# Performance work log

Measured on AMD Instinct MI355X. Metric: run time of the kernel, lower is better.

Reference implementation:

```python
import jax, jax.numpy as jnp
import numpy as np

N_NODES = 50000
N_EDGES = 1600000
NEG_SLOPE = 0.2


def setup_inputs() -> dict:
    key = jax.random.key(0)
    ks = jax.random.split(key, 11)
    s = 0.1  # small init scale
    return {
        "x": jax.random.normal(ks[0], (N_NODES, 128), dtype=jnp.float32),
        "edge_index": jax.random.randint(ks[1], (2, N_EDGES), 0, N_NODES, dtype=jnp.int64),
        "W1": jax.random.normal(ks[2], (128, 128), dtype=jnp.float32) * s,
        "att_src1": jax.random.normal(ks[3], (2, 64), dtype=jnp.float32) * s,
        "att_dst1": jax.random.normal(ks[4], (2, 64), dtype=jnp.float32) * s,
        "b1": jax.random.normal(ks[5], (128,), dtype=jnp.float32) * s,
        "W2": jax.random.normal(ks[6], (128, 64), dtype=jnp.float32) * s,
        "att_src2": jax.random.normal(ks[7], (1, 64), dtype=jnp.float32) * s,
        "att_dst2": jax.random.normal(ks[8], (1, 64), dtype=jnp.float32) * s,
        "b2": jax.random.normal(ks[9], (64,), dtype=jnp.float32) * s,
    }


def gat_conv(x, W, a_src, a_dst, bias, src, dst, n_nodes):
    # x: [N, F_in]; W: [F_in, H*C]; a_src/a_dst: [H, C]; bias: [H*C]
    H, C = a_src.shape
    xl = (x @ W).reshape(n_nodes, H, C)                 # [N,H,C]
    alpha_s = jnp.einsum('nhc,hc->nh', xl, a_src)       # [N,H]
    alpha_d = jnp.einsum('nhc,hc->nh', xl, a_dst)       # [N,H]
    e = jax.nn.leaky_relu(alpha_s[src] + alpha_d[dst], NEG_SLOPE)  # [E,H]
    # segment softmax over edges sharing the same destination node
    m = jax.ops.segment_max(e, dst, num_segments=n_nodes)          # [N,H]
    m = jnp.where(jnp.isfinite(m), m, 0.0)
    e = jnp.exp(e - m[dst])
    denom = jax.ops.segment_sum(e, dst, num_segments=n_nodes)      # [N,H]
    alpha = e / denom[dst]                               # self-loops guarantee denom > 0
    msg = xl[src] * alpha[:, :, None]                    # [E,H,C]
    out = jax.ops.segment_sum(msg, dst, num_segments=n_nodes)      # [N,H,C]
    return out.reshape(n_nodes, H * C) + bias


def reference(x, edge_index, W1, att_src1, att_dst1, b1, W2, att_src2, att_dst2, b2):
    n = x.shape[0]
    # PyG GATConv default add_self_loops=True
    loops = jnp.arange(n, dtype=edge_index.dtype)
    src = jnp.concatenate([edge_index[0], loops])
    dst = jnp.concatenate([edge_index[1], loops])

    h = gat_conv(x, W1, att_src1, att_dst1, b1, src, dst, n)   # [N, 128]
    h = jax.nn.relu(h)                                          # dropout p=0 (eval)
    h = gat_conv(h, W2, att_src2, att_dst2, b2, src, dst, n)   # [N, 64]
    h = jax.nn.relu(h)
    return h
```

## Files before the change

### kernel.cpp

```cpp
#include <hip/hip_runtime.h>
#include <cstdint>
#include <cstddef>

#define NEG_SLOPE 0.2f

#define NB 128
#define LOG_NB 7
#define MAXK 512

__device__ inline unsigned short f2bf(float f) {
    unsigned int u = __float_as_uint(f);
    u += 0x7FFFu + ((u >> 16) & 1u);
    return (unsigned short)(u >> 16);
}
__device__ inline float bf_lo(unsigned int u) { return __uint_as_float(u << 16); }
__device__ inline float bf_hi(unsigned int u) { return __uint_as_float(u & 0xFFFF0000u); }

__global__ __launch_bounds__(256) void sort_count_kernel(const int* __restrict__ ei, int E,
                                                         int K, int CH, int* __restrict__ bcnt) {
    __shared__ int hist[4 * MAXK];
    int tid = threadIdx.x;
    int wiw = tid >> 6;
    for (int i = tid; i < K; i += 256) {
        hist[i] = 0; hist[MAXK + i] = 0; hist[2 * MAXK + i] = 0; hist[3 * MAXK + i] = 0;
    }
    __syncthreads();
    int lo = blockIdx.x * CH;
    int hi = lo + CH; if (hi > E) hi = E;
    for (int e = lo + tid; e < hi; e += 256)
        atomicAdd(&hist[wiw * MAXK + (ei[(size_t)E + e] >> LOG_NB)], 1);
    __syncthreads();
    for (int i = tid; i < K; i += 256) {
        int c = hist[i] + hist[MAXK + i] + hist[2 * MAXK + i] + hist[3 * MAXK + i];
        if (c) atomicAdd(&bcnt[i], c);
    }
}

__global__ void sort_scan_kernel(const int* __restrict__ bcnt, int* __restrict__ boff,
                                 int* __restrict__ bcur, int K, int E) {
    __shared__ int buf[MAXK];
    int tid = threadIdx.x;
    int v = (tid < K) ? bcnt[tid] : 0;
    buf[tid] = v;
    __syncthreads();
    for (int o = 1; o < MAXK; o <<= 1) {
        int t = (tid >= o) ? buf[tid - o] : 0;
        __syncthreads();
        buf[tid] += t;
        __syncthreads();
    }
    if (tid < K) {
        int ex = buf[tid] - v;
        boff[tid] = ex;
        bcur[tid] = ex;
    }
    if (tid == K) boff[K] = E;
}


template <int FOUT, int H, int ROWS>
__device__ __forceinline__ void gemm_att_body(const float* __restrict__ X,
                                              const float* __restrict__ W,
                                              const float* __restrict__ attS,
                                              const float* __restrict__ attD,
                                              unsigned short* __restrict__ Ybf,
                                              float* __restrict__ as_,
                                              float* __restrict__ ad_, int N, int bid,
                                              float* sX, float* sW) {
    constexpr int CG  = FOUT / 4;
    constexpr int RR  = (ROWS * FOUT) / 1024;
    constexpr int LDX = 36;
    int tid = threadIdx.x;
    int rowbase = bid * ROWS;
    int cg = tid % CG;
    int rg = tid / CG;
    int r0 = rg * RR;

    float acc[RR][4];
#pragma unroll
    for (int i = 0; i < RR; i++)
#pragma unroll
        for (int c = 0; c < 4; c++) acc[i][c] = 0.f;

    for (int k0 = 0; k0 < 128; k0 += 32) {
        __syncthreads();
        for (int idx = tid; idx < ROWS * 8; idx += 256) {
            int r = idx >> 3, q = idx & 7;
            int row = rowbase + r;
            float4 val = (row < N) ? *(const float4*)&X[(size_t)row * 128 + k0 + q * 4]
                                   : make_float4(0.f, 0.f, 0.f, 0.f);
            *(float4*)&sX[r * LDX + q * 4] = val;
        }
        for (int idx = tid; idx < 8 * FOUT; idx += 256)
            *(float4*)&sW[idx * 4] = *(const float4*)&W[(size_t)k0 * FOUT + idx * 4];
        __syncthreads();
        for (int k = 0; k < 32; k += 4) {
            float4 xr[RR];
#pragma unroll
            for (int i = 0; i < RR; i++)
                xr[i] = *(const float4*)&sX[(r0 + i) * LDX + k];
#pragma unroll
            for (int kk = 0; kk < 4; kk++) {
                float4 wv = ((const float4*)(sW + (size_t)(k + kk) * FOUT))[cg];
#pragma unroll
                for (int i = 0; i < RR; i++) {
                    float xv = (&xr[i].x)[kk];
                    acc[i][0] = fmaf(xv, wv.x, acc[i][0]);
                    acc[i][1] = fmaf(xv, wv.y, acc[i][1]);
                    acc[i][2] = fmaf(xv, wv.z, acc[i][2]);
                    acc[i][3] = fmaf(xv, wv.w, acc[i][3]);
                }
            }
        }
    }

#pragma unroll
    for (int i = 0; i < RR; i++) {
        int row = rowbase + r0 + i;
        if (row < N) {
            ushort4 v;
            v.x = f2bf(acc[i][0]); v.y = f2bf(acc[i][1]);
            v.z = f2bf(acc[i][2]); v.w = f2bf(acc[i][3]);
            *(ushort4*)(Ybf + (size_t)row * FOUT + cg * 4) = v;
        }
    }

    float4 asv = ((const float4*)attS)[cg];
    float4 adv = ((const float4*)attD)[cg];
    int head = (H == 2) ? (cg >> 4) : 0;
#pragma unroll
    for (int i = 0; i < RR; i++) {
        float ps = acc[i][0] * asv.x + acc[i][1] * asv.y + acc[i][2] * asv.z + acc[i][3] * asv.w;
        float pd = acc[i][0] * adv.x + acc[i][1] * adv.y + acc[i][2] * adv.z + acc[i][3] * adv.w;
#pragma unroll
        for (int o = 1; o <= 8; o <<= 1) { ps += __shfl_xor(ps, o); pd += __shfl_xor(pd, o); }
        int row = rowbase + r0 + i;
        if ((tid & 15) == 0 && row < N) {
            as_[(size_t)row * H + head] = ps;
            ad_[(size_t)row * H + head] = pd;
        }
    }
}

__global__ __launch_bounds__(256) void scatter_gemm1_kernel(const int* __restrict__ ei, int E,
                                                            int K, int CH, int* __restrict__ bcur,
                                                            unsigned int* __restrict__ bkt,
                                                            const float* __restrict__ X,
                                                            const float* __restrict__ W1,
                                                            const float* __restrict__ attS,
                                                            const float* __restrict__ attD,
                                                            unsigned short* __restrict__ Ybf,
                                                            float* __restrict__ as_,
                                                            float* __restrict__ ad_, int N, int G) {
    __shared__ float sX[64 * 36];
    __shared__ float sW[32 * 128];
    if (blockIdx.x < G) {
        int* hist = (int*)sX;
        int* base = (int*)sW;
        int* cur2 = (int*)sW + MAXK;
        int tid = threadIdx.x;
        int wiw = tid >> 6;
        for (int i = tid; i < K; i += 256) {
            hist[i] = 0; hist[MAXK + i] = 0; hist[2 * MAXK + i] = 0; hist[3 * MAXK + i] = 0;
        }
        __syncthreads();
        int lo = blockIdx.x * CH;
        int hi = lo + CH; if (hi > E) hi = E;
        for (int e = lo + tid; e < hi; e += 256)
            atomicAdd(&hist[wiw * MAXK + (ei[(size_t)E + e] >> LOG_NB)], 1);
        __syncthreads();
        for (int i = tid; i < K; i += 256) {
            int c = hist[i] + hist[MAXK + i] + hist[2 * MAXK + i] + hist[3 * MAXK + i];
            base[i] = c ? atomicAdd(&bcur[i], c) : 0;
            cur2[i] = 0;
        }
        __syncthreads();
        for (int e = lo + tid; e < hi; e += 256) {
            int s = ei[e];
            int d = ei[(size_t)E + e];
            int k = d >> LOG_NB;
            int r = atomicAdd(&cur2[k], 1);
            bkt[(size_t)base[k] + r] = (unsigned int)s | ((unsigned int)d << 16);
        }
    } else {
        gemm_att_body<128, 2, 64>(X, W1, attS, attD, Ybf, as_, ad_, N, blockIdx.x - G, sX, sW);
    }
}

__global__ __launch_bounds__(256) void gemm2_kernel(const float* __restrict__ X,
                                                    const float* __restrict__ W,
                                                    const float* __restrict__ attS,
                                                    const float* __restrict__ attD,
                                                    unsigned short* __restrict__ Ybf,
                                                    float* __restrict__ as_,
                                                    float* __restrict__ ad_, int N) {
    __shared__ float sX[64 * 36];
    __shared__ float sW[32 * 64];
    gemm_att_body<64, 1, 64>(X, W, attS, attD, Ybf, as_, ad_, N, blockIdx.x, sX, sW);
}

__global__ __launch_bounds__(256) void sort_finalize_kernel(const unsigned int* __restrict__ bkt,
                                                            const int* __restrict__ boff,
                                                            int* __restrict__ off,
                                                            unsigned int* __restrict__ csrc, int N) {
    __shared__ int nhist[4 * NB];
    __shared__ int part[256];
    __shared__ int loff[NB];
    int k = blockIdx.x;
    int tid = threadIdx.x;
    int wiw = tid >> 6;
    int node0 = k << LOG_NB;
    int nh = N - node0; if (nh > NB) nh = NB;
    int beg = boff[k], end = boff[k + 1];
    for (int i = tid; i < NB; i += 256) {
        nhist[i] = 0; nhist[NB + i] = 0; nhist[2 * NB + i] = 0; nhist[3 * NB + i] = 0;
    }
    __syncthreads();
    for (int e = beg + tid; e < end; e += 256)
        atomicAdd(&nhist[wiw * NB + ((bkt[e] >> 16) - node0)], 1);
    __syncthreads();
    int i0 = 2 * tid, i1 = 2 * tid + 1;
    int v0 = (i0 < nh) ? nhist[i0] + nhist[NB + i0] + nhist[2 * NB + i0] + nhist[3 * NB + i0] + 1 : 0;
    int v1 = (i1 < nh) ? nhist[i1] + nhist[NB + i1] + nhist[2 * NB + i1] + nhist[3 * NB + i1] + 1 : 0;
    part[tid] = v0 + v1;
    __syncthreads();
    for (int o = 1; o < 256; o <<= 1) {
        int t = (tid >= o) ? part[tid - o] : 0;
        __syncthreads();
        part[tid] += t;
        __syncthreads();
    }
    int gbase = beg + node0;
    int base = gbase + ((tid > 0) ? part[tid - 1] : 0);
    if (i0 < nh) loff[i0] = base;
    if (i1 < nh) loff[i1] = base + v0;
    __syncthreads();
    for (int i = tid; i < nh; i += 256) {
        int node = node0 + i;
        off[node] = loff[i];
        csrc[loff[i]] = (unsigned int)node | ((unsigned int)node << 16);
        nhist[i] = loff[i] + 1;
    }
    if (node0 + nh == N && tid == 0) off[N] = gbase + part[255];
    __syncthreads();
    for (int e = beg + tid; e < end; e += 256) {
        unsigned int p = bkt[e];
        int pos = atomicAdd(&nhist[(p >> 16) - node0], 1);
        csrc[pos] = p;
    }
}


__global__ __launch_bounds__(256) void agg1_kernel(const unsigned short* __restrict__ xl,
                                                   const float* __restrict__ as_,
                                                   const float* __restrict__ ad_,
                                                   const float* __restrict__ bias,
                                                   const int* __restrict__ off,
                                                   const unsigned int* __restrict__ csrc,
                                                   float* __restrict__ out, int N) {
    __shared__ float4 sps[4][64];
    int wiw  = threadIdx.x >> 6;
    int lane = threadIdx.x & 63;
    int node = blockIdx.x * 4 + wiw;
    if (node >= N) return;
    int beg = off[node], end = off[node + 1];
    int deg = end - beg;
    float2 adn = ((const float2*)ad_)[node];

    int cl  = lane & 15;
    int sub = lane >> 4;
    int hd1 = (cl >> 3) & 1;
    float acc[8];
#pragma unroll
    for (int i = 0; i < 8; i++) acc[i] = 0.f;
    const char* xbase = (const char*)xl + cl * 16;

    if (deg <= 64) {
        int so = 0;
        float t0 = -1e30f, t1 = -1e30f;
        if (lane < deg) {
            int s = (int)(csrc[beg + lane] & 0xFFFFu);
            so = s << 8;
            float2 asv = ((const float2*)as_)[s];
            t0 = asv.x + adn.x; t0 = t0 > 0.f ? t0 : NEG_SLOPE * t0;
            t1 = asv.y + adn.y; t1 = t1 > 0.f ? t1 : NEG_SLOPE * t1;
        }
        float m0 = t0, m1 = t1;
#pragma unroll
        for (int o = 32; o; o >>= 1) {
            m0 = fmaxf(m0, __shfl_xor(m0, o));
            m1 = fmaxf(m1, __shfl_xor(m1, o));
        }
        float e0 = (lane < deg) ? __expf(t0 - m0) : 0.f;
        float e1 = (lane < deg) ? __expf(t1 - m1) : 0.f;
        float s0 = e0, s1 = e1;
#pragma unroll
        for (int o = 32; o; o >>= 1) { s0 += __shfl_xor(s0, o); s1 += __shfl_xor(s1, o); }
        sps[wiw][lane] = make_float4(e0 / s0, e1 / s1, __int_as_float(so), 0.f);
        int iters = (deg + 3) >> 2;
#pragma unroll 8
        for (int j = 0; j < iters; j++) {
            float4 q = sps[wiw][j * 4 + sub];
            float a  = hd1 ? q.y : q.x;
            uint4 v  = *(const uint4*)(xbase + __float_as_int(q.z));
            acc[0] = fmaf(a, bf_lo(v.x), acc[0]); acc[1] = fmaf(a, bf_hi(v.x), acc[1]);
            acc[2] = fmaf(a, bf_lo(v.y), acc[2]); acc[3] = fmaf(a, bf_hi(v.y), acc[3]);
            acc[4] = fmaf(a, bf_lo(v.z), acc[4]); acc[5] = fmaf(a, bf_hi(v.z), acc[5]);
            acc[6] = fmaf(a, bf_lo(v.w), acc[6]); acc[7] = fmaf(a, bf_hi(v.w), acc[7]);
        }
    } else {
        float m0 = -1e30f, m1 = -1e30f;
        for (int b = beg; b < end; b += 64) {
            int e = b + lane;
            if (e < end) {
                int s = (int)(csrc[e] & 0xFFFFu);
                float2 asv = ((const float2*)as_)[s];
                float t0 = asv.x + adn.x; t0 = t0 > 0.f ? t0 : NEG_SLOPE * t0;
                float t1 = asv.y + adn.y; t1 = t1 > 0.f ? t1 : NEG_SLOPE * t1;
                m0 = fmaxf(m0, t0); m1 = fmaxf(m1, t1);
            }
        }
#pragma unroll
        for (int o = 32; o; o >>= 1) {
            m0 = fmaxf(m0, __shfl_xor(m0, o));
            m1 = fmaxf(m1, __shfl_xor(m1, o));
        }
        float s0 = 0.f, s1 = 0.f;
        for (int b = beg; b < end; b += 64) {
            int e = b + lane;
            if (e < end) {
                int s = (int)(csrc[e] & 0xFFFFu);
                float2 asv = ((const float2*)as_)[s];
                float t0 = asv.x + adn.x; t0 = t0 > 0.f ? t0 : NEG_SLOPE * t0;
                float t1 = asv.y + adn.y; t1 = t1 > 0.f ? t1 : NEG_SLOPE * t1;
                s0 += __expf(t0 - m0); s1 += __expf(t1 - m1);
            }
        }
#pragma unroll
        for (int o = 32; o; o >>= 1) { s0 += __shfl_xor(s0, o); s1 += __shfl_xor(s1, o); }
        float i0 = 1.f / s0, i1 = 1.f / s1;
        for (int b = beg; b < end; b += 64) {
            int cnt = end - b; if (cnt > 64) cnt = 64;
            float p0 = 0.f, p1 = 0.f; int so = 0;
            if (lane < cnt) {
                int s = (int)(csrc[b + lane] & 0xFFFFu);
                so = s << 8;
                float2 asv = ((const float2*)as_)[s];
                float t0 = asv.x + adn.x; t0 = t0 > 0.f ? t0 : NEG_SLOPE * t0;
                float t1 = asv.y + adn.y; t1 = t1 > 0.f ? t1 : NEG_SLOPE * t1;
                p0 = __expf(t0 - m0) * i0; p1 = __expf(t1 - m1) * i1;
            }
            sps[wiw][lane] = make_float4(p0, p1, __int_as_float(so), 0.f);
            int iters = (cnt + 3) >> 2;
#pragma unroll 8
            for (int j = 0; j < iters; j++) {
                float4 q = sps[wiw][j * 4 + sub];
                float a  = hd1 ? q.y : q.x;
                uint4 v  = *(const uint4*)(xbase + __float_as_int(q.z));
                acc[0] = fmaf(a, bf_lo(v.x), acc[0]); acc[1] = fmaf(a, bf_hi(v.x), acc[1]);
                acc[2] = fmaf(a, bf_lo(v.y), acc[2]); acc[3] = fmaf(a, bf_hi(v.y), acc[3]);
                acc[4] = fmaf(a, bf_lo(v.z), acc[4]); acc[5] = fmaf(a, bf_hi(v.z), acc[5]);
                acc[6] = fmaf(a, bf_lo(v.w), acc[6]); acc[7] = fmaf(a, bf_hi(v.w), acc[7]);
            }
        }
    }
#pragma unroll
    for (int o = 16; o <= 32; o <<= 1)
#pragma unroll
        for (int i = 0; i < 8; i++) acc[i] += __shfl_xor(acc[i], o);
    if (sub == 0) {
        float* op = out + (size_t)node * 128 + cl * 8;
        const float* bp = bias + cl * 8;
#pragma unroll
        for (int i = 0; i < 8; i++) op[i] = fmaxf(acc[i] + bp[i], 0.f);
    }
}


__global__ __launch_bounds__(256) void agg2_kernel(const unsigned short* __restrict__ xl,
                                                   const float* __restrict__ as_,
                                                   const float* __restrict__ ad_,
                                                   const float* __restrict__ bias,
                                                   const int* __restrict__ off,
                                                   const unsigned int* __restrict__ csrc,
                                                   float* __restrict__ out, int N) {
    __shared__ float2 sps[4][64];
    int wiw  = threadIdx.x >> 6;
    int lane = threadIdx.x & 63;
    int node = blockIdx.x * 4 + wiw;
    if (node >= N) return;
    int beg = off[node], end = off[node + 1];
    int deg = end - beg;
    float adn = ad_[node];

    int cl  = lane & 7;
    int sub = lane >> 3;
    float acc[8];
#pragma unroll
    for (int i = 0; i < 8; i++) acc[i] = 0.f;
    const char* xbase = (const char*)xl + cl * 16;

    if (deg <= 64) {
        int so = 0;
        float t = -1e30f;
        if (lane < deg) {
            int s = (int)(csrc[beg + lane] & 0xFFFFu);
            so = s << 7;
            t = as_[s] + adn;
            t = t > 0.f ? t : NEG_SLOPE * t;
        }
        float m = t;
#pragma unroll
        for (int o = 32; o; o >>= 1) m = fmaxf(m, __shfl_xor(m, o));
        float evv = (lane < deg) ? __expf(t - m) : 0.f;
        float sum = evv;
#pragma unroll
        for (int o = 32; o; o >>= 1) sum += __shfl_xor(sum, o);
        sps[wiw][lane] = make_float2(evv / sum, __int_as_float(so));
        int iters = (deg + 7) >> 3;
#pragma unroll 8
        for (int j = 0; j < iters; j++) {
            float2 q = sps[wiw][j * 8 + sub];
            float a  = q.x;
            uint4 v  = *(const uint4*)(xbase + __float_as_int(q.y));
            acc[0] = fmaf(a, bf_lo(v.x), acc[0]); acc[1] = fmaf(a, bf_hi(v.x), acc[1]);
            acc[2] = fmaf(a, bf_lo(v.y), acc[2]); acc[3] = fmaf(a, bf_hi(v.y), acc[3]);
            acc[4] = fmaf(a, bf_lo(v.z), acc[4]); acc[5] = fmaf(a, bf_hi(v.z), acc[5]);
            acc[6] = fmaf(a, bf_lo(v.w), acc[6]); acc[7] = fmaf(a, bf_hi(v.w), acc[7]);
        }
    } else {
        float m = -1e30f;
        for (int b = beg; b < end; b += 64) {
            int e = b + lane;
            if (e < end) {
                float t = as_[csrc[e] & 0xFFFFu] + adn;
                t = t > 0.f ? t : NEG_SLOPE * t;
                m = fmaxf(m, t);
            }
        }
#pragma unroll
        for (int o = 32; o; o >>= 1) m = fmaxf(m, __shfl_xor(m, o));
        float sum = 0.f;
        for (int b = beg; b < end; b += 64) {
            int e = b + lane;
            if (e < end) {
                float t = as_[csrc[e] & 0xFFFFu] + adn;
                t = t > 0.f ? t : NEG_SLOPE * t;
                sum += __expf(t - m);
            }
        }
#pragma unroll
        for (int o = 32; o; o >>= 1) sum += __shfl_xor(sum, o);
        float inv = 1.f / sum;
        for (int b = beg; b < end; b += 64) {
            int cnt = end - b; if (cnt > 64) cnt = 64;
            float p = 0.f; int so = 0;
            if (lane < cnt) {
                int s = (int)(csrc[b + lane] & 0xFFFFu);
                so = s << 7;
                float t = as_[s] + adn;
                t = t > 0.f ? t : NEG_SLOPE * t;
                p = __expf(t - m) * inv;
            }
            sps[wiw][lane] = make_float2(p, __int_as_float(so));
            int iters = (cnt + 7) >> 3;
#pragma unroll 8
            for (int j = 0; j < iters; j++) {
                float2 q = sps[wiw][j * 8 + sub];
                float a  = q.x;
                uint4 v  = *(const uint4*)(xbase + __float_as_int(q.y));
                acc[0] = fmaf(a, bf_lo(v.x), acc[0]); acc[1] = fmaf(a, bf_hi(v.x), acc[1]);
                acc[2] = fmaf(a, bf_lo(v.y), acc[2]); acc[3] = fmaf(a, bf_hi(v.y), acc[3]);
                acc[4] = fmaf(a, bf_lo(v.z), acc[4]); acc[5] = fmaf(a, bf_hi(v.z), acc[5]);
                acc[6] = fmaf(a, bf_lo(v.w), acc[6]); acc[7] = fmaf(a, bf_hi(v.w), acc[7]);
            }
        }
    }
#pragma unroll
    for (int o = 8; o <= 32; o <<= 1)
#pragma unroll
        for (int i = 0; i < 8; i++) acc[i] += __shfl_xor(acc[i], o);
    if (sub == 0) {
        float* op = out + (size_t)node * 64 + cl * 8;
        const float* bp = bias + cl * 8;
#pragma unroll
        for (int i = 0; i < 8; i++) op[i] = fmaxf(acc[i] + bp[i], 0.f);
    }
}


extern "C" void kernel_launch(void* const* d_in, const int* in_sizes, int n_in,
                              void* d_out, int out_size, void* d_ws, size_t ws_size,
                              hipStream_t stream) {
    const float* x        = (const float*)d_in[0];
    const int*   ei       = (const int*)d_in[1];
    const float* W1       = (const float*)d_in[2];
    const float* attS1    = (const float*)d_in[3];
    const float* attD1    = (const float*)d_in[4];
    const float* b1       = (const float*)d_in[5];
    const float* W2       = (const float*)d_in[6];
    const float* attS2    = (const float*)d_in[7];
    const float* attD2    = (const float*)d_in[8];
    const float* b2       = (const float*)d_in[9];
    float* out            = (float*)d_out;

    int N  = in_sizes[0] / 128;
    int E  = in_sizes[1] / 2;
    int EE = E + N;
    int K  = (N + NB - 1) >> LOG_NB;

    char* w = (char*)d_ws;
    auto alloc = [&](size_t bytes) -> void* {
        void* p = (void*)w;
        w += (bytes + 255) & ~(size_t)255;
        return p;
    };
    int*   bcnt = (int*)alloc((size_t)(K + 1) * 4);
    int*   boff = (int*)alloc((size_t)(K + 1) * 4);
    int*   bcur = (int*)alloc((size_t)(K + 1) * 4);
    int*   off  = (int*)alloc((size_t)(N + 1) * 4);
    unsigned int* csrc = (unsigned int*)alloc((size_t)EE * 4);
    unsigned int* bkt  = (unsigned int*)alloc((size_t)E * 4);
    unsigned short* xl1 = (unsigned short*)alloc((size_t)N * 128 * 2);
    float* sd1  = (float*)alloc((size_t)N * 2 * 4);
    float* dd1  = (float*)alloc((size_t)N * 2 * 4);
    float* h1   = (float*)alloc((size_t)N * 128 * 4);

    unsigned short* xl2 = xl1;
    float* sd2 = sd1;
    float* dd2 = dd1;

    hipMemsetAsync(bcnt, 0, (size_t)(K + 1) * 4, stream);

    int G   = 256;
    int CH  = (E + G - 1) / G;
    int GB1 = (N + 63) / 64;
    sort_count_kernel<<<G, 256, 0, stream>>>(ei, E, K, CH, bcnt);
    sort_scan_kernel<<<1, MAXK, 0, stream>>>(bcnt, boff, bcur, K, E);
    scatter_gemm1_kernel<<<G + GB1, 256, 0, stream>>>(ei, E, K, CH, bcur, bkt,
                                                      x, W1, attS1, attD1, xl1, sd1, dd1, N, G);
    sort_finalize_kernel<<<K, 256, 0, stream>>>(bkt, boff, off, csrc, N);

    agg1_kernel<<<(N + 3) / 4, 256, 0, stream>>>(xl1, sd1, dd1, b1, off, csrc, h1, N);

    gemm2_kernel<<<(N + 63) / 64, 256, 0, stream>>>(h1, W2, attS2, attD2, xl2, sd2, dd2, N);
    agg2_kernel<<<(N + 3) / 4, 256, 0, stream>>>(xl2, sd2, dd2, b2, off, csrc, out, N);
}
```

Measured before the change: 298.9 us.

## Process four destination nodes per wavefront with batched softmax prologue loads

New measurement: 321.0 us. +7.4%, slower.

```diff
diff --git a/kernel.cpp b/kernel.cpp
--- a/kernel.cpp
+++ b/kernel.cpp
@@ -250,6 +250,12 @@
     }
 }
 
+#define FMA8(a, v)                                                                       \
+    acc[0] = fmaf(a, bf_lo((v).x), acc[0]); acc[1] = fmaf(a, bf_hi((v).x), acc[1]);      \
+    acc[2] = fmaf(a, bf_lo((v).y), acc[2]); acc[3] = fmaf(a, bf_hi((v).y), acc[3]);      \
+    acc[4] = fmaf(a, bf_lo((v).z), acc[4]); acc[5] = fmaf(a, bf_hi((v).z), acc[5]);      \
+    acc[6] = fmaf(a, bf_lo((v).w), acc[6]); acc[7] = fmaf(a, bf_hi((v).w), acc[7]);
+
 
 __global__ __launch_bounds__(256) void agg1_kernel(const unsigned short* __restrict__ xl,
                                                    const float* __restrict__ as_,
@@ -258,32 +264,46 @@
                                                    const int* __restrict__ off,
                                                    const unsigned int* __restrict__ csrc,
                                                    float* __restrict__ out, int N) {
-    __shared__ float4 sps[4][64];
+    __shared__ float4 sps[4][4][64];
     int wiw  = threadIdx.x >> 6;
     int lane = threadIdx.x & 63;
-    int node = blockIdx.x * 4 + wiw;
-    if (node >= N) return;
-    int beg = off[node], end = off[node + 1];
-    int deg = end - beg;
-    float2 adn = ((const float2*)ad_)[node];
+    int node0 = blockIdx.x * 16 + wiw * 4;
+    if (node0 >= N) return;
 
     int cl  = lane & 15;
     int sub = lane >> 4;
     int hd1 = (cl >> 3) & 1;
-    float acc[8];
-#pragma unroll
-    for (int i = 0; i < 8; i++) acc[i] = 0.f;
     const char* xbase = (const char*)xl + cl * 16;
 
-    if (deg <= 64) {
-        int so = 0;
+    int begk[4], degk[4];
+#pragma unroll
+    for (int k = 0; k < 4; k++) {
+        int node = node0 + k;
+        if (node < N) { int b = off[node]; begk[k] = b; degk[k] = off[node + 1] - b; }
+        else          { begk[k] = 0; degk[k] = 0; }
+    }
+    float2 adnk[4];
+#pragma unroll
+    for (int k = 0; k < 4; k++) {
+        int node = node0 + k;
+        adnk[k] = (node < N) ? ((const float2*)ad_)[node] : make_float2(0.f, 0.f);
+    }
+    int sk[4];
+#pragma unroll
+    for (int k = 0; k < 4; k++)
+        sk[k] = (degk[k] <= 64 && lane < degk[k]) ? (int)(csrc[begk[k] + lane] & 0xFFFFu) : 0;
+    float2 asvk[4];
+#pragma unroll
+    for (int k = 0; k < 4; k++)
+        asvk[k] = ((const float2*)as_)[sk[k]];
+
+#pragma unroll
+    for (int k = 0; k < 4; k++) {
+        if (degk[k] == 0 || degk[k] > 64) continue;
         float t0 = -1e30f, t1 = -1e30f;
-        if (lane < deg) {
-            int s = (int)(csrc[beg + lane] & 0xFFFFu);
-            so = s << 8;
-            float2 asv = ((const float2*)as_)[s];
-            t0 = asv.x + adn.x; t0 = t0 > 0.f ? t0 : NEG_SLOPE * t0;
-            t1 = asv.y + adn.y; t1 = t1 > 0.f ? t1 : NEG_SLOPE * t1;
+        if (lane < degk[k]) {
+            t0 = asvk[k].x + adnk[k].x; t0 = t0 > 0.f ? t0 : NEG_SLOPE * t0;
+            t1 = asvk[k].y + adnk[k].y; t1 = t1 > 0.f ? t1 : NEG_SLOPE * t1;
         }
         float m0 = t0, m1 = t1;
 #pragma unroll
@@ -291,88 +311,95 @@
             m0 = fmaxf(m0, __shfl_xor(m0, o));
             m1 = fmaxf(m1, __shfl_xor(m1, o));
         }
-        float e0 = (lane < deg) ? __expf(t0 - m0) : 0.f;
-        float e1 = (lane < deg) ? __expf(t1 - m1) : 0.f;
+        float e0 = (lane < degk[k]) ? __expf(t0 - m0) : 0.f;
+        float e1 = (lane < degk[k]) ? __expf(t1 - m1) : 0.f;
         float s0 = e0, s1 = e1;
 #pragma unroll
         for (int o = 32; o; o >>= 1) { s0 += __shfl_xor(s0, o); s1 += __shfl_xor(s1, o); }
-        sps[wiw][lane] = make_float4(e0 / s0, e1 / s1, __int_as_float(so), 0.f);
-        int iters = (deg + 3) >> 2;
-#pragma unroll 8
-        for (int j = 0; j < iters; j++) {
-            float4 q = sps[wiw][j * 4 + sub];
-            float a  = hd1 ? q.y : q.x;
-            uint4 v  = *(const uint4*)(xbase + __float_as_int(q.z));
-            acc[0] = fmaf(a, bf_lo(v.x), acc[0]); acc[1] = fmaf(a, bf_hi(v.x), acc[1]);
-            acc[2] = fmaf(a, bf_lo(v.y), acc[2]); acc[3] = fmaf(a, bf_hi(v.y), acc[3]);
-            acc[4] = fmaf(a, bf_lo(v.z), acc[4]); acc[5] = fmaf(a, bf_hi(v.z), acc[5]);
-            acc[6] = fmaf(a, bf_lo(v.w), acc[6]); acc[7] = fmaf(a, bf_hi(v.w), acc[7]);
-        }
-    } else {
-        float m0 = -1e30f, m1 = -1e30f;
-        for (int b = beg; b < end; b += 64) {
-            int e = b + lane;
-            if (e < end) {
-                int s = (int)(csrc[e] & 0xFFFFu);
-                float2 asv = ((const float2*)as_)[s];
-                float t0 = asv.x + adn.x; t0 = t0 > 0.f ? t0 : NEG_SLOPE * t0;
-                float t1 = asv.y + adn.y; t1 = t1 > 0.f ? t1 : NEG_SLOPE * t1;
-                m0 = fmaxf(m0, t0); m1 = fmaxf(m1, t1);
-            }
-        }
-#pragma unroll
-        for (int o = 32; o; o >>= 1) {
-            m0 = fmaxf(m0, __shfl_xor(m0, o));
-            m1 = fmaxf(m1, __shfl_xor(m1, o));
-        }
-        float s0 = 0.f, s1 = 0.f;
-        for (int b = beg; b < end; b += 64) {
-            int e = b + lane;
-            if (e < end) {
-                int s = (int)(csrc[e] & 0xFFFFu);
-                float2 asv = ((const float2*)as_)[s];
-                float t0 = asv.x + adn.x; t0 = t0 > 0.f ? t0 : NEG_SLOPE * t0;
-                float t1 = asv.y + adn.y; t1 = t1 > 0.f ? t1 : NEG_SLOPE * t1;
-                s0 += __expf(t0 - m0); s1 += __expf(t1 - m1);
-            }
-        }
-#pragma unroll
-        for (int o = 32; o; o >>= 1) { s0 += __shfl_xor(s0, o); s1 += __shfl_xor(s1, o); }
-        float i0 = 1.f / s0, i1 = 1.f / s1;
-        for (int b = beg; b < end; b += 64) {
-            int cnt = end - b; if (cnt > 64) cnt = 64;
-            float p0 = 0.f, p1 = 0.f; int so = 0;
-            if (lane < cnt) {
-                int s = (int)(csrc[b + lane] & 0xFFFFu);
-                so = s << 8;
-                float2 asv = ((const float2*)as_)[s];
-                float t0 = asv.x + adn.x; t0 = t0 > 0.f ? t0 : NEG_SLOPE * t0;
-                float t1 = asv.y + adn.y; t1 = t1 > 0.f ? t1 : NEG_SLOPE * t1;
-                p0 = __expf(t0 - m0) * i0; p1 = __expf(t1 - m1) * i1;
-            }
-            sps[wiw][lane] = make_float4(p0, p1, __int_as_float(so), 0.f);
-            int iters = (cnt + 3) >> 2;
+        sps[wiw][k][lane] = make_float4(e0 / s0, e1 / s1, __int_as_float(sk[k] << 8), 0.f);
+    }
+
+#pragma unroll
+    for (int k = 0; k < 4; k++) {
+        int node = node0 + k;
+        if (node >= N) break;
+        float acc[8];
+#pragma unroll
+        for (int i = 0; i < 8; i++) acc[i] = 0.f;
+
+        if (degk[k] <= 64) {
+            int iters = (degk[k] + 3) >> 2;
 #pragma unroll 8
             for (int j = 0; j < iters; j++) {
-                float4 q = sps[wiw][j * 4 + sub];
+                float4 q = sps[wiw][k][j * 4 + sub];
                 float a  = hd1 ? q.y : q.x;
                 uint4 v  = *(const uint4*)(xbase + __float_as_int(q.z));
-                acc[0] = fmaf(a, bf_lo(v.x), acc[0]); acc[1] = fmaf(a, bf_hi(v.x), acc[1]);
-                acc[2] = fmaf(a, bf_lo(v.y), acc[2]); acc[3] = fmaf(a, bf_hi(v.y), acc[3]);
-                acc[4] = fmaf(a, bf_lo(v.z), acc[4]); acc[5] = fmaf(a, bf_hi(v.z), acc[5]);
-                acc[6] = fmaf(a, bf_lo(v.w), acc[6]); acc[7] = fmaf(a, bf_hi(v.w), acc[7]);
-            }
-        }
-    }
-#pragma unroll
-    for (int o = 16; o <= 32; o <<= 1)
-#pragma unroll
-        for (int i = 0; i < 8; i++) acc[i] += __shfl_xor(acc[i], o);
-    if (sub == 0) {
-        float* op = out + (size_t)node * 128 + cl * 8;
-        const float* bp = bias + cl * 8;
-#pragma unroll
-        for (int i = 0; i < 8; i++) op[i] = fmaxf(acc[i] + bp[i], 0.f);
+                FMA8(a, v)
+            }
+        } else {
+            int beg = begk[k], end = beg + degk[k];
+            float m0 = -1e30f, m1 = -1e30f;
+            for (int b = beg; b < end; b += 64) {
+                int e = b + lane;
+                if (e < end) {
+                    int s = (int)(csrc[e] & 0xFFFFu);
+                    float2 asv = ((const float2*)as_)[s];
+                    float t0 = asv.x + adnk[k].x; t0 = t0 > 0.f ? t0 : NEG_SLOPE * t0;
+                    float t1 = asv.y + adnk[k].y; t1 = t1 > 0.f ? t1 : NEG_SLOPE * t1;
+                    m0 = fmaxf(m0, t0); m1 = fmaxf(m1, t1);
+                }
+            }
+#pragma unroll
+            for (int o = 32; o; o >>= 1) {
+                m0 = fmaxf(m0, __shfl_xor(m0, o));
+                m1 = fmaxf(m1, __shfl_xor(m1, o));
+            }
+            float s0 = 0.f, s1 = 0.f;
+            for (int b = beg; b < end; b += 64) {
+                int e = b + lane;
+                if (e < end) {
+                    int s = (int)(csrc[e] & 0xFFFFu);
+                    float2 asv = ((const float2*)as_)[s];
+                    float t0 = asv.x + adnk[k].x; t0 = t0 > 0.f ? t0 : NEG_SLOPE * t0;
+                    float t1 = asv.y + adnk[k].y; t1 = t1 > 0.f ? t1 : NEG_SLOPE * t1;
+                    s0 += __expf(t0 - m0); s1 += __expf(t1 - m1);
+                }
+            }
+#pragma unroll
+            for (int o = 32; o; o >>= 1) { s0 += __shfl_xor(s0, o); s1 += __shfl_xor(s1, o); }
+            float i0 = 1.f / s0, i1 = 1.f / s1;
+            for (int b = beg; b < end; b += 64) {
+                int cnt = end - b; if (cnt > 64) cnt = 64;
+                float p0 = 0.f, p1 = 0.f; int so = 0;
+                if (lane < cnt) {
+                    int s = (int)(csrc[b + lane] & 0xFFFFu);
+                    so = s << 8;
+                    float2 asv = ((const float2*)as_)[s];
+                    float t0 = asv.x + adnk[k].x; t0 = t0 > 0.f ? t0 : NEG_SLOPE * t0;
+                    float t1 = asv.y + adnk[k].y; t1 = t1 > 0.f ? t1 : NEG_SLOPE * t1;
+                    p0 = __expf(t0 - m0) * i0; p1 = __expf(t1 - m1) * i1;
+                }
+                sps[wiw][k][lane] = make_float4(p0, p1, __int_as_float(so), 0.f);
+                int iters = (cnt + 3) >> 2;
+#pragma unroll 8
+                for (int j = 0; j < iters; j++) {
+                    float4 q = sps[wiw][k][j * 4 + sub];
+                    float a  = hd1 ? q.y : q.x;
+                    uint4 v  = *(const uint4*)(xbase + __float_as_int(q.z));
+                    FMA8(a, v)
+                }
+            }
+        }
+#pragma unroll
+        for (int o = 16; o <= 32; o <<= 1)
+#pragma unroll
+            for (int i = 0; i < 8; i++) acc[i] += __shfl_xor(acc[i], o);
+        if (sub == 0) {
+            float* op = out + (size_t)node * 128 + cl * 8;
+            const float* bp = bias + cl * 8;
+#pragma unroll
+            for (int i = 0; i < 8; i++) op[i] = fmaxf(acc[i] + bp[i], 0.f);
+        }
     }
 }
 
@@ -384,107 +411,129 @@
                                                    const int* __restrict__ off,
                                                    const unsigned int* __restrict__ csrc,
                                                    float* __restrict__ out, int N) {
-    __shared__ float2 sps[4][64];
+    __shared__ float2 sps[4][4][64];
     int wiw  = threadIdx.x >> 6;
     int lane = threadIdx.x & 63;
-    int node = blockIdx.x * 4 + wiw;
-    if (node >= N) return;
-    int beg = off[node], end = off[node + 1];
-    int deg = end - beg;
-    float adn = ad_[node];
+    int node0 = blockIdx.x * 16 + wiw * 4;
+    if (node0 >= N) return;
 
     int cl  = lane & 7;
     int sub = lane >> 3;
-    float acc[8];
-#pragma unroll
-    for (int i = 0; i < 8; i++) acc[i] = 0.f;
     const char* xbase = (const char*)xl + cl * 16;
 
-    if (deg <= 64) {
-        int so = 0;
+    int begk[4], degk[4];
+#pragma unroll
+    for (int k = 0; k < 4; k++) {
+        int node = node0 + k;
+        if (node < N) { int b = off[node]; begk[k] = b; degk[k] = off[node + 1] - b; }
+        else          { begk[k] = 0; degk[k] = 0; }
+    }
+    float adnk[4];
+#pragma unroll
+    for (int k = 0; k < 4; k++) {
+        int node = node0 + k;
+        adnk[k] = (node < N) ? ad_[node] : 0.f;
+    }
+    int sk[4];
+#pragma unroll
+    for (int k = 0; k < 4; k++)
+        sk[k] = (degk[k] <= 64 && lane < degk[k]) ? (int)(csrc[begk[k] + lane] & 0xFFFFu) : 0;
+    float asvk[4];
+#pragma unroll
+    for (int k = 0; k < 4; k++)
+        asvk[k] = as_[sk[k]];
+
+#pragma unroll
+    for (int k = 0; k < 4; k++) {
+        if (degk[k] == 0 || degk[k] > 64) continue;
         float t = -1e30f;
-        if (lane < deg) {
-            int s = (int)(csrc[beg + lane] & 0xFFFFu);
-            so = s << 7;
-            t = as_[s] + adn;
+        if (lane < degk[k]) {
+            t = asvk[k] + adnk[k];
             t = t > 0.f ? t : NEG_SLOPE * t;
         }
         float m = t;
 #pragma unroll
         for (int o = 32; o; o >>= 1) m = fmaxf(m, __shfl_xor(m, o));
-        float evv = (lane < deg) ? __expf(t - m) : 0.f;
+        float evv = (lane < degk[k]) ? __expf(t - m) : 0.f;
         float sum = evv;
 #pragma unroll
         for (int o = 32; o; o >>= 1) sum += __shfl_xor(sum, o);
-        sps[wiw][lane] = make_float2(evv / sum, __int_as_float(so));
-        int iters = (deg + 7) >> 3;
-#pragma unroll 8
-        for (int j = 0; j < iters; j++) {
-            float2 q = sps[wiw][j * 8 + sub];
-            float a  = q.x;
-            uint4 v  = *(const uint4*)(xbase + __float_as_int(q.y));
-            acc[0] = fmaf(a, bf_lo(v.x), acc[0]); acc[1] = fmaf(a, bf_hi(v.x), acc[1]);
-            acc[2] = fmaf(a, bf_lo(v.y), acc[2]); acc[3] = fmaf(a, bf_hi(v.y), acc[3]);
-            acc[4] = fmaf(a, bf_lo(v.z), acc[4]); acc[5] = fmaf(a, bf_hi(v.z), acc[5]);
-            acc[6] = fmaf(a, bf_lo(v.w), acc[6]); acc[7] = fmaf(a, bf_hi(v.w), acc[7]);
-        }
-    } else {
-        float m = -1e30f;
-        for (int b = beg; b < end; b += 64) {
-            int e = b + lane;
-            if (e < end) {
-                float t = as_[csrc[e] & 0xFFFFu] + adn;
-                t = t > 0.f ? t : NEG_SLOPE * t;
-                m = fmaxf(m, t);
-            }
-        }
-#pragma unroll
-        for (int o = 32; o; o >>= 1) m = fmaxf(m, __shfl_xor(m, o));
-        float sum = 0.f;
-        for (int b = beg; b < end; b += 64) {
-            int e = b + lane;
-            if (e < end) {
-                float t = as_[csrc[e] & 0xFFFFu] + adn;
-                t = t > 0.f ? t : NEG_SLOPE * t;
-                sum += __expf(t - m);
-            }
-        }
-#pragma unroll
-        for (int o = 32; o; o >>= 1) sum += __shfl_xor(sum, o);
-        float inv = 1.f / sum;
-        for (int b = beg; b < end; b += 64) {
-            int cnt = end - b; if (cnt > 64) cnt = 64;
-            float p = 0.f; int so = 0;
-            if (lane < cnt) {
-                int s = (int)(csrc[b + lane] & 0xFFFFu);
-                so = s << 7;
-                float t = as_[s] + adn;
-                t = t > 0.f ? t : NEG_SLOPE * t;
-                p = __expf(t - m) * inv;
-            }
-            sps[wiw][lane] = make_float2(p, __int_as_float(so));
-            int iters = (cnt + 7) >> 3;
+        sps[wiw][k][lane] = make_float2(evv / sum, __int_as_float(sk[k] << 7));
+    }
+
+#pragma unroll
+    for (int k = 0; k < 4; k++) {
+        int node = node0 + k;
+        if (node >= N) break;
+        float acc[8];
+#pragma unroll
+        for (int i = 0; i < 8; i++) acc[i] = 0.f;
+
+        if (degk[k] <= 64) {
+            int iters = (degk[k] + 7) >> 3;
 #pragma unroll 8
             for (int j = 0; j < iters; j++) {
-                float2 q = sps[wiw][j * 8 + sub];
+                float2 q = sps[wiw][k][j * 8 + sub];
                 float a  = q.x;
                 uint4 v  = *(const uint4*)(xbase + __float_as_int(q.y));
-                acc[0] = fmaf(a, bf_lo(v.x), acc[0]); acc[1] = fmaf(a, bf_hi(v.x), acc[1]);
-                acc[2] = fmaf(a, bf_lo(v.y), acc[2]); acc[3] = fmaf(a, bf_hi(v.y), acc[3]);
-                acc[4] = fmaf(a, bf_lo(v.z), acc[4]); acc[5] = fmaf(a, bf_hi(v.z), acc[5]);
-                acc[6] = fmaf(a, bf_lo(v.w), acc[6]); acc[7] = fmaf(a, bf_hi(v.w), acc[7]);
-            }
-        }
-    }
-#pragma unroll
-    for (int o = 8; o <= 32; o <<= 1)
-#pragma unroll
-        for (int i = 0; i < 8; i++) acc[i] += __shfl_xor(acc[i], o);
-    if (sub == 0) {
-        float* op = out + (size_t)node * 64 + cl * 8;
-        const float* bp = bias + cl * 8;
-#pragma unroll
-        for (int i = 0; i < 8; i++) op[i] = fmaxf(acc[i] + bp[i], 0.f);
+                FMA8(a, v)
+            }
+        } else {
+            int beg = begk[k], end = beg + degk[k];
+            float m = -1e30f;
+            for (int b = beg; b < end; b += 64) {
+                int e = b + lane;
+                if (e < end) {
+                    float t = as_[csrc[e] & 0xFFFFu] + adnk[k];
+                    t = t > 0.f ? t : NEG_SLOPE * t;
+                    m = fmaxf(m, t);
+                }
+            }
+#pragma unroll
+            for (int o = 32; o; o >>= 1) m = fmaxf(m, __shfl_xor(m, o));
+            float sum = 0.f;
+            for (int b = beg; b < end; b += 64) {
+                int e = b + lane;
+                if (e < end) {
+                    float t = as_[csrc[e] & 0xFFFFu] + adnk[k];
+                    t = t > 0.f ? t : NEG_SLOPE * t;
+                    sum += __expf(t - m);
+                }
+            }
+#pragma unroll
+            for (int o = 32; o; o >>= 1) sum += __shfl_xor(sum, o);
+            float inv = 1.f / sum;
+            for (int b = beg; b < end; b += 64) {
+                int cnt = end - b; if (cnt > 64) cnt = 64;
+                float p = 0.f; int so = 0;
+                if (lane < cnt) {
+                    int s = (int)(csrc[b + lane] & 0xFFFFu);
+                    so = s << 7;
+                    float t = as_[s] + adnk[k];
+                    t = t > 0.f ? t : NEG_SLOPE * t;
+                    p = __expf(t - m) * inv;
+                }
+                sps[wiw][k][lane] = make_float2(p, __int_as_float(so));
+                int iters = (cnt + 7) >> 3;
+#pragma unroll 8
+                for (int j = 0; j < iters; j++) {
+                    float2 q = sps[wiw][k][j * 8 + sub];
+                    float a  = q.x;
+                    uint4 v  = *(const uint4*)(xbase + __float_as_int(q.y));
+                    FMA8(a, v)
+                }
+            }
+        }
+#pragma unroll
+        for (int o = 8; o <= 32; o <<= 1)
+#pragma unroll
+            for (int i = 0; i < 8; i++) acc[i] += __shfl_xor(acc[i], o);
+        if (sub == 0) {
+            float* op = out + (size_t)node * 64 + cl * 8;
+            const float* bp = bias + cl * 8;
+#pragma unroll
+            for (int i = 0; i < 8; i++) op[i] = fmaxf(acc[i] + bp[i], 0.f);
+        }
     }
 }
 
@@ -541,8 +590,8 @@
                                                       x, W1, attS1, attD1, xl1, sd1, dd1, N, G);
     sort_finalize_kernel<<<K, 256, 0, stream>>>(bkt, boff, off, csrc, N);
 
-    agg1_kernel<<<(N + 3) / 4, 256, 0, stream>>>(xl1, sd1, dd1, b1, off, csrc, h1, N);
+    agg1_kernel<<<(N + 15) / 16, 256, 0, stream>>>(xl1, sd1, dd1, b1, off, csrc, h1, N);
 
     gemm2_kernel<<<(N + 63) / 64, 256, 0, stream>>>(h1, W2, attS2, attD2, xl2, sd2, dd2, N);
-    agg2_kernel<<<(N + 3) / 4, 256, 0, stream>>>(xl2, sd2, dd2, b2, off, csrc, out, N);
-}
+    agg2_kernel<<<(N + 15) / 16, 256, 0, stream>>>(xl2, sd2, dd2, b2, off, csrc, out, N);
+}
```
